# Optimization experiments

Measured on AMD Instinct MI355X. Metric: run time of the kernel, lower is better.

Reference implementation:

```python
import jax, jax.numpy as jnp
import numpy as np

N = 20000      # num nodes
E = 320000     # num edges
F = 128        # num_features
NUM_RBF = 20   # Message.num_atoms (hardcoded in torch source)
CUTOFF = 5.0


def setup_inputs() -> dict:
    key = jax.random.key(0)
    ks = jax.random.split(key, 12)
    node_s = jax.random.normal(ks[0], (N, F), dtype=jnp.float32)
    node_vec = jax.random.normal(ks[1], (N, F, 3), dtype=jnp.float32)
    edge = jax.random.randint(ks[2], (E, 2), 0, N, dtype=jnp.int32)
    edge_difference = jax.random.normal(ks[3], (E, 3), dtype=jnp.float32)
    # distances strictly positive and mostly inside cutoff (rbf divides by dist)
    edge_dis = jax.random.uniform(ks[4], (E,), dtype=jnp.float32, minval=0.5, maxval=CUTOFF * 1.1)
    s = 1.0 / np.sqrt(F)
    W1 = jax.random.normal(ks[5], (F, F), dtype=jnp.float32) * s
    b1 = jnp.zeros((F,), dtype=jnp.float32)
    W2 = jax.random.normal(ks[6], (F, 3 * F), dtype=jnp.float32) * s
    b2 = jnp.zeros((3 * F,), dtype=jnp.float32)
    Wf = jax.random.normal(ks[7], (NUM_RBF, 3 * F), dtype=jnp.float32) / np.sqrt(NUM_RBF)
    bf = jnp.zeros((3 * F,), dtype=jnp.float32)
    return {"node_s": node_s, "node_vec": node_vec, "edge": edge,
            "edge_difference": edge_difference, "edge_dis": edge_dis,
            "W1": W1, "b1": b1, "W2": W2, "b2": b2, "Wf": Wf, "bf": bf}


def reference(node_s, node_vec, edge, edge_difference, edge_dis, W1, b1, W2, b2, Wf, bf):
    src = edge[:, 1]  # gather index (neighbor j)
    dst = edge[:, 0]  # scatter index (center i)
    inv_d = 1.0 / edge_dis[:, None]                                   # [E,1]
    n = jnp.arange(1, NUM_RBF + 1, dtype=edge_dis.dtype)              # [20]
    rbf_feat = jnp.sin((n * (jnp.pi / CUTOFF)) * edge_dis[:, None]) * inv_d  # [E,20]
    filt = rbf_feat @ Wf + bf                                         # [E,3F]
    ccut = jnp.where(edge_dis <= CUTOFF,
                     0.5 * (jnp.cos(jnp.pi * edge_dis / CUTOFF) + 1.0), 0.0)  # [E]
    # faithful to torch: both filter and cutoff are re-indexed by edge[:,1]
    filter_W = filt[src] * ccut[src][:, None]                         # [E,3F]
    h = jax.nn.silu(node_s @ W1 + b1)                                 # [N,F]
    s_out = h @ W2 + b2                                               # [N,3F]
    filer_output = filter_W * s_out[src]                              # [E,3F]
    gate_state, gate_edge, message_scalar = jnp.split(filer_output, 3, axis=1)
    message_vec = node_vec[src] * gate_state[:, :, None]              # [E,F,3]
    # edge_vec in the torch source is dead code (never used) -> omitted
    temp_s = jnp.zeros_like(node_s).at[dst].add(message_scalar)       # [N,F]
    temp_vec = jnp.zeros_like(node_vec).at[dst].add(message_vec)      # [N,F,3]
    return (node_vec + temp_vec, node_s + temp_s)
```

## Files before the change

### kernel.cpp

```cpp
#include <hip/hip_runtime.h>
#include <hip/hip_bf16.h>

#define FDIM 128
#define NRBF 20
#define PI_OVER_CUT 0.6283185307179586f

#define WCONV_ELEMS (128 * 128 + 256 * 128 + 256 * 32)
#define WCONV_BLOCKS (WCONV_ELEMS / 256)

#define DEG_CAP 64

typedef short bf8_t __attribute__((ext_vector_type(8)));
typedef float f4_t  __attribute__((ext_vector_type(4)));
typedef unsigned short us8_t __attribute__((ext_vector_type(8)));

static __device__ __forceinline__ unsigned short bf16_bits(float x) {
    unsigned u = __float_as_uint(x);
    unsigned r = u + 0x7FFF + ((u >> 16) & 1);
    return (unsigned short)(r >> 16);
}
static __device__ __forceinline__ float bf16_f(unsigned short b) {
    return __uint_as_float(((unsigned)b) << 16);
}

__global__ __launch_bounds__(256) void prep_kernel(
    const float* __restrict__ W1, const float* __restrict__ W2,
    const float* __restrict__ Wf,
    unsigned short* __restrict__ W1T, unsigned short* __restrict__ W2T,
    unsigned short* __restrict__ WfT,
    int* __restrict__ cursor, int N)
{
    int b = blockIdx.x;
    if (b < WCONV_BLOCKS) {
        int i = b * 256 + threadIdx.x;
        if (i < 128 * 128) {
            int n = i >> 7, k = i & 127;
            W1T[n * 128 + k] = bf16_bits(W1[k * 128 + n]);
        } else if (i < 128 * 128 + 256 * 128) {
            int j = i - 128 * 128;
            int n = j >> 7, k = j & 127;
            int col = (n < 128) ? n : n + 128;
            W2T[n * 128 + k] = bf16_bits(W2[k * 384 + col]);
        } else {
            int j = i - (128 * 128 + 256 * 128);
            int n = j >> 5, k = j & 31;
            int col = (n < 128) ? n : n + 128;
            WfT[n * 32 + k] = (k < NRBF) ? bf16_bits(Wf[k * 384 + col])
                                         : (unsigned short)0;
        }
    } else {
        int i = (b - WCONV_BLOCKS) * 256 + threadIdx.x;
        if (i < N) cursor[i] = 0;
    }
}

__global__ __launch_bounds__(256) void node_fused(
    const float* __restrict__ S, const float* __restrict__ node_vec,
    const float* __restrict__ edge_dis,
    const unsigned short* __restrict__ W1T, const float* __restrict__ b1,
    const unsigned short* __restrict__ W2T, const float* __restrict__ b2,
    const unsigned short* __restrict__ WfT, const float* __restrict__ bfv,
    ushort4* __restrict__ VM, int N,
    const int* __restrict__ edge, int* __restrict__ cursor,
    int* __restrict__ src_pad, int E, int nodeBlocks)
{
    if (blockIdx.x >= nodeBlocks) {
        int i = (blockIdx.x - nodeBlocks) * 256 + threadIdx.x;
        if (i < E) {
            int d = edge[2 * i];
            int s = edge[2 * i + 1];
            int pos = atomicAdd(&cursor[d], 1);
            src_pad[((size_t)d << 6) + pos] = s;
        }
        return;
    }

    __shared__ __align__(16) unsigned short sh_s[16][136];
    __shared__ __align__(16) unsigned short sh_h[16][136];
    __shared__ __align__(16) unsigned short sh_rbf[16][40];
    __shared__ __align__(16) float sh_nv[16][388];
    __shared__ float sh_ccut[16];

    const int tid  = threadIdx.x;
    const int lane = tid & 63;
    const int wave = tid >> 6;
    const int l15  = lane & 15;
    const int quad = lane >> 4;
    const int m0   = blockIdx.x * 16;

    for (int t = tid; t < 16 * 32; t += 256) {
        int row = t >> 5, c4 = (t & 31) * 4;
        int n = m0 + row; if (n >= N) n = N - 1;
        float4 x = *(const float4*)(S + (size_t)n * FDIM + c4);
        ushort4 u;
        u.x = bf16_bits(x.x); u.y = bf16_bits(x.y);
        u.z = bf16_bits(x.z); u.w = bf16_bits(x.w);
        *(ushort4*)&sh_s[row][c4] = u;
    }
    for (int t = tid; t < 16 * 96; t += 256) {
        int row = t / 96, i4 = (t % 96) * 4;
        int n = m0 + row; if (n >= N) n = N - 1;
        *(float4*)&sh_nv[row][i4] =
            *(const float4*)(node_vec + (size_t)n * 384 + i4);
    }
    if (tid < 16 * 8) {
        int row = tid >> 3, k0 = (tid & 7) * 4;
        int n = m0 + row; if (n >= N) n = N - 1;
        float dd = edge_dis[n];
        float ph = PI_OVER_CUT * dd;
        float inv = 1.0f / dd;
        ushort4 u;
        u.x = (k0 + 0 < NRBF) ? bf16_bits(sinf((float)(k0 + 1) * ph) * inv) : 0;
        u.y = (k0 + 1 < NRBF) ? bf16_bits(sinf((float)(k0 + 2) * ph) * inv) : 0;
        u.z = (k0 + 2 < NRBF) ? bf16_bits(sinf((float)(k0 + 3) * ph) * inv) : 0;
        u.w = (k0 + 3 < NRBF) ? bf16_bits(sinf((float)(k0 + 4) * ph) * inv) : 0;
        *(ushort4*)&sh_rbf[row][k0] = u;
    }
    if (tid < 16) {
        int n = m0 + tid; if (n >= N) n = N - 1;
        float dd = edge_dis[n];
        sh_ccut[tid] = (dd <= 5.0f) ? 0.5f * (cosf(PI_OVER_CUT * dd) + 1.0f) : 0.0f;
    }
    __syncthreads();

    {
        bf8_t a1[4];
        #pragma unroll
        for (int kk = 0; kk < 4; kk++)
            a1[kk] = *(const bf8_t*)&sh_s[l15][kk * 32 + quad * 8];

        #pragma unroll
        for (int i = 0; i < 2; i++) {
            int col = (wave * 2 + i) * 16 + l15;
            const unsigned short* wp = W1T + (size_t)col * FDIM + quad * 8;
            f4_t acc = {0.f, 0.f, 0.f, 0.f};
            #pragma unroll
            for (int kk = 0; kk < 4; kk++) {
                bf8_t b = *(const bf8_t*)(wp + kk * 32);
                acc = __builtin_amdgcn_mfma_f32_16x16x32_bf16(a1[kk], b, acc, 0, 0, 0);
            }
            float bb = b1[col];
            #pragma unroll
            for (int r = 0; r < 4; r++) {
                float x = acc[r] + bb;
                x = x / (1.f + expf(-x));
                sh_h[quad * 4 + r][col] = bf16_bits(x);
            }
        }
    }
    __syncthreads();

    bf8_t a2[4], af;
    #pragma unroll
    for (int kk = 0; kk < 4; kk++)
        a2[kk] = *(const bf8_t*)&sh_h[l15][kk * 32 + quad * 8];
    af = *(const bf8_t*)&sh_rbf[l15][quad * 8];

    #pragma unroll
    for (int i = 0; i < 2; i++) {
        int pc = (wave * 2 + i) * 16 + l15;
        const unsigned short* wg = W2T + (size_t)pc * FDIM + quad * 8;
        const unsigned short* wm = W2T + (size_t)(pc + 128) * FDIM + quad * 8;
        f4_t ag = {0.f, 0.f, 0.f, 0.f}, am = {0.f, 0.f, 0.f, 0.f};
        #pragma unroll
        for (int kk = 0; kk < 4; kk++) {
            bf8_t bg = *(const bf8_t*)(wg + kk * 32);
            bf8_t bm = *(const bf8_t*)(wm + kk * 32);
            ag = __builtin_amdgcn_mfma_f32_16x16x32_bf16(a2[kk], bg, ag, 0, 0, 0);
            am = __builtin_amdgcn_mfma_f32_16x16x32_bf16(a2[kk], bm, am, 0, 0, 0);
        }
        f4_t fg = {0.f, 0.f, 0.f, 0.f}, fm = {0.f, 0.f, 0.f, 0.f};
        {
            bf8_t bg = *(const bf8_t*)(WfT + (size_t)pc * 32 + quad * 8);
            bf8_t bm = *(const bf8_t*)(WfT + (size_t)(pc + 128) * 32 + quad * 8);
            fg = __builtin_amdgcn_mfma_f32_16x16x32_bf16(af, bg, fg, 0, 0, 0);
            fm = __builtin_amdgcn_mfma_f32_16x16x32_bf16(af, bm, fm, 0, 0, 0);
        }

        float b2g = b2[pc], b2m = b2[256 + pc];
        float bfg = bfv[pc], bfm = bfv[256 + pc];
        #pragma unroll
        for (int r = 0; r < 4; r++) {
            int lrow = quad * 4 + r;
            int n = m0 + lrow;
            if (n < N) {
                float cc = sh_ccut[lrow];
                float a  = (fg[r] + bfg) * cc * (ag[r] + b2g);
                float mv = (fm[r] + bfm) * cc * (am[r] + b2m);
                const float* vp = &sh_nv[lrow][3 * pc];
                ushort4 rec;
                rec.x = bf16_bits(a * vp[0]);
                rec.y = bf16_bits(a * vp[1]);
                rec.z = bf16_bits(a * vp[2]);
                rec.w = bf16_bits(mv);
                VM[(size_t)n * FDIM + pc] = rec;
            }
        }
    }
}

__global__ __launch_bounds__(256) void gather_bf16(
    const int* __restrict__ cursor, const int* __restrict__ src_pad,
    const us8_t* __restrict__ VM8, const float* __restrict__ node_vec,
    const float* __restrict__ node_s,
    float* __restrict__ out_vec, float* __restrict__ out_s, int N)
{
    const int lane = threadIdx.x & 63;
    const int nw = gridDim.x * 4;
    for (int d = blockIdx.x * 4 + (threadIdx.x >> 6); d < N; d += nw) {
        int beg = d << 6;
        int end = beg + cursor[d];

        float a0A = 0.f, a1A = 0.f, a2A = 0.f, asA = 0.f;
        float a0B = 0.f, a1B = 0.f, a2B = 0.f, asB = 0.f;

        int j = beg;
        for (; j + 7 < end; j += 8) {
            us8_t r0 = VM8[(size_t)src_pad[j]     * 64 + lane];
            us8_t r1 = VM8[(size_t)src_pad[j + 1] * 64 + lane];
            us8_t r2 = VM8[(size_t)src_pad[j + 2] * 64 + lane];
            us8_t r3 = VM8[(size_t)src_pad[j + 3] * 64 + lane];
            us8_t r4 = VM8[(size_t)src_pad[j + 4] * 64 + lane];
            us8_t r5 = VM8[(size_t)src_pad[j + 5] * 64 + lane];
            us8_t r6 = VM8[(size_t)src_pad[j + 6] * 64 + lane];
            us8_t r7 = VM8[(size_t)src_pad[j + 7] * 64 + lane];
            #define ACC(r) \
                a0A += bf16_f(r[0]); a1A += bf16_f(r[1]); a2A += bf16_f(r[2]); asA += bf16_f(r[3]); \
                a0B += bf16_f(r[4]); a1B += bf16_f(r[5]); a2B += bf16_f(r[6]); asB += bf16_f(r[7]);
            ACC(r0) ACC(r1) ACC(r2) ACC(r3) ACC(r4) ACC(r5) ACC(r6) ACC(r7)
        }
        for (; j + 3 < end; j += 4) {
            us8_t r0 = VM8[(size_t)src_pad[j]     * 64 + lane];
            us8_t r1 = VM8[(size_t)src_pad[j + 1] * 64 + lane];
            us8_t r2 = VM8[(size_t)src_pad[j + 2] * 64 + lane];
            us8_t r3 = VM8[(size_t)src_pad[j + 3] * 64 + lane];
            ACC(r0) ACC(r1) ACC(r2) ACC(r3)
        }
        for (; j < end; j++) {
            us8_t r = VM8[(size_t)src_pad[j] * 64 + lane];
            ACC(r)
            #undef ACC
        }

        {
            const float* sp = node_s + (size_t)d * FDIM + 2 * lane;
            float* op = out_s + (size_t)d * FDIM + 2 * lane;
            float2 ns = *(const float2*)sp;
            float2 r; r.x = ns.x + asA; r.y = ns.y + asB;
            *(float2*)op = r;
        }
        {
            const float* ip = node_vec + (size_t)d * 384 + 6 * lane;
            float* op = out_vec + (size_t)d * 384 + 6 * lane;
            op[0] = ip[0] + a0A;
            op[1] = ip[1] + a1A;
            op[2] = ip[2] + a2A;
            op[3] = ip[3] + a0B;
            op[4] = ip[4] + a1B;
            op[5] = ip[5] + a2B;
        }
    }
}

extern "C" void kernel_launch(void* const* d_in, const int* in_sizes, int n_in,
                              void* d_out, int out_size, void* d_ws, size_t ws_size,
                              hipStream_t stream) {
    const float* node_s   = (const float*)d_in[0];
    const float* node_vec = (const float*)d_in[1];
    const int*   edge     = (const int*)d_in[2];
    const float* edge_dis = (const float*)d_in[4];
    const float* W1 = (const float*)d_in[5];
    const float* b1 = (const float*)d_in[6];
    const float* W2 = (const float*)d_in[7];
    const float* b2 = (const float*)d_in[8];
    const float* Wf = (const float*)d_in[9];
    const float* bf = (const float*)d_in[10];

    const int N = in_sizes[0] / FDIM;
    const int E = in_sizes[2] / 2;

    float* out_vec = (float*)d_out;
    float* out_s   = out_vec + (size_t)N * 384;

    int* cursor  = (int*)d_ws;
    int* src_pad = cursor + N;
    size_t int_bytes = (((size_t)N * (DEG_CAP + 1) * 4) + 15) & ~(size_t)15;
    unsigned short* W1T = (unsigned short*)((char*)d_ws + int_bytes);
    unsigned short* W2T = W1T + 128 * 128;
    unsigned short* WfT = W2T + 256 * 128;
    ushort4*        VMh = (ushort4*)(WfT + 256 * 32);

    const int zeroBlocks = (N + 255) / 256;
    prep_kernel<<<WCONV_BLOCKS + zeroBlocks, 256, 0, stream>>>(
        W1, W2, Wf, W1T, W2T, WfT, cursor, N);

    const int nodeBlocks = (N + 15) / 16;
    const int edgeBlocks = (E + 255) / 256;
    node_fused<<<nodeBlocks + edgeBlocks, 256, 0, stream>>>(
        node_s, node_vec, edge_dis, W1T, b1, W2T, b2, WfT, bf, VMh, N,
        edge, cursor, src_pad, E, nodeBlocks);

    int gblocks = (N + 3) / 4;
    if (gblocks > 2048) gblocks = 2048;
    gather_bf16<<<gblocks, 256, 0, stream>>>(
        cursor, src_pad, (const us8_t*)VMh, node_vec, node_s,
        out_vec, out_s, N);
}
```

Baseline: 198.5 us.

## Schedule edge bucketing blocks first, 4 edges per thread, drop node_vec LDS staging

Moves the edge-bucketing blocks to the front of the fused launch so their atomics start early and overlap with the node MFMA blocks. Each bucketing thread now handles four edges with int2 loads, which cuts the number of blocks. The node_vec shared-memory staging is removed and values are read straight from global memory in the epilogue. This lowers LDS use and may raise occupancy, at the cost of strided global reads of node_vec.

```diff
diff --git a/kernel.cpp b/kernel.cpp
--- a/kernel.cpp
+++ b/kernel.cpp
@@ -9,6 +9,8 @@
 #define WCONV_BLOCKS (WCONV_ELEMS / 256)
 
 #define DEG_CAP 64
+
+#define EPB 1024
 
 typedef short bf8_t __attribute__((ext_vector_type(8)));
 typedef float f4_t  __attribute__((ext_vector_type(4)));
@@ -62,15 +64,18 @@
     const unsigned short* __restrict__ WfT, const float* __restrict__ bfv,
     ushort4* __restrict__ VM, int N,
     const int* __restrict__ edge, int* __restrict__ cursor,
-    int* __restrict__ src_pad, int E, int nodeBlocks)
+    int* __restrict__ src_pad, int E, int edgeBlocks)
 {
-    if (blockIdx.x >= nodeBlocks) {
-        int i = (blockIdx.x - nodeBlocks) * 256 + threadIdx.x;
-        if (i < E) {
-            int d = edge[2 * i];
-            int s = edge[2 * i + 1];
-            int pos = atomicAdd(&cursor[d], 1);
-            src_pad[((size_t)d << 6) + pos] = s;
+    if (blockIdx.x < edgeBlocks) {
+        int base = blockIdx.x * EPB;
+        #pragma unroll
+        for (int it = 0; it < 4; it++) {
+            int i = base + it * 256 + threadIdx.x;
+            if (i < E) {
+                int2 e = ((const int2*)edge)[i];
+                int pos = atomicAdd(&cursor[e.x], 1);
+                src_pad[((size_t)e.x << 6) + pos] = e.y;
+            }
         }
         return;
     }
@@ -78,7 +83,6 @@
     __shared__ __align__(16) unsigned short sh_s[16][136];
     __shared__ __align__(16) unsigned short sh_h[16][136];
     __shared__ __align__(16) unsigned short sh_rbf[16][40];
-    __shared__ __align__(16) float sh_nv[16][388];
     __shared__ float sh_ccut[16];
 
     const int tid  = threadIdx.x;
@@ -86,7 +90,7 @@
     const int wave = tid >> 6;
     const int l15  = lane & 15;
     const int quad = lane >> 4;
-    const int m0   = blockIdx.x * 16;
+    const int m0   = (blockIdx.x - edgeBlocks) * 16;
 
     for (int t = tid; t < 16 * 32; t += 256) {
         int row = t >> 5, c4 = (t & 31) * 4;
@@ -96,12 +100,6 @@
         u.x = bf16_bits(x.x); u.y = bf16_bits(x.y);
         u.z = bf16_bits(x.z); u.w = bf16_bits(x.w);
         *(ushort4*)&sh_s[row][c4] = u;
-    }
-    for (int t = tid; t < 16 * 96; t += 256) {
-        int row = t / 96, i4 = (t % 96) * 4;
-        int n = m0 + row; if (n >= N) n = N - 1;
-        *(float4*)&sh_nv[row][i4] =
-            *(const float4*)(node_vec + (size_t)n * 384 + i4);
     }
     if (tid < 16 * 8) {
         int row = tid >> 3, k0 = (tid & 7) * 4;
@@ -187,7 +185,7 @@
                 float cc = sh_ccut[lrow];
                 float a  = (fg[r] + bfg) * cc * (ag[r] + b2g);
                 float mv = (fm[r] + bfm) * cc * (am[r] + b2m);
-                const float* vp = &sh_nv[lrow][3 * pc];
+                const float* vp = node_vec + (size_t)n * 384 + 3 * pc;
                 ushort4 rec;
                 rec.x = bf16_bits(a * vp[0]);
                 rec.y = bf16_bits(a * vp[1]);
@@ -295,10 +293,10 @@
         W1, W2, Wf, W1T, W2T, WfT, cursor, N);
 
     const int nodeBlocks = (N + 15) / 16;
-    const int edgeBlocks = (E + 255) / 256;
-    node_fused<<<nodeBlocks + edgeBlocks, 256, 0, stream>>>(
+    const int edgeBlocks = (E + EPB - 1) / EPB;
+    node_fused<<<edgeBlocks + nodeBlocks, 256, 0, stream>>>(
         node_s, node_vec, edge_dis, W1T, b1, W2T, b2, WfT, bf, VMh, N,
-        edge, cursor, src_pad, E, nodeBlocks);
+        edge, cursor, src_pad, E, edgeBlocks);
 
     int gblocks = (N + 3) / 4;
     if (gblocks > 2048) gblocks = 2048;
```

New measurement: 194.8 us. No clear change (-1.9%).
